# Performance work log

Measured on AMD Instinct MI355X. Metric: run time of the kernel, lower is better.

Reference implementation:

```python
import jax, jax.numpy as jnp
import numpy as np

B, T, H, C = 64, 2048, 128, 7


def _lstm_layer(xs, W_ih, W_hh, b):
    # xs: [T, B, H_in]; PyTorch gate order i, f, g, o
    Bsz = xs.shape[1]
    Hs = W_hh.shape[1]

    def step(carry, x_t):
        h, c = carry
        gates = x_t @ W_ih.T + h @ W_hh.T + b  # [B, 4H]
        i, f, g, o = jnp.split(gates, 4, axis=-1)
        c = jax.nn.sigmoid(f) * c + jax.nn.sigmoid(i) * jnp.tanh(g)
        h = jax.nn.sigmoid(o) * jnp.tanh(c)
        return (h, c), h

    init = (jnp.zeros((Bsz, Hs), xs.dtype), jnp.zeros((Bsz, Hs), xs.dtype))
    _, ys = jax.lax.scan(step, init, xs)
    return ys  # [T, B, H]


def setup_inputs() -> dict:
    key = jax.random.key(0)
    ks = jax.random.split(key, 12)
    s = 1.0 / np.sqrt(H)
    u = lambda k, shape: jax.random.uniform(k, shape, jnp.float32, -s, s)
    x = jax.random.normal(ks[0], (B, T, 1), jnp.float32)
    lengths = jax.random.randint(ks[1], (B,), 1, T + 1, jnp.int32)
    return {
        "x": x,
        "lengths": lengths,
        "ff_w": u(ks[2], (H, 1)),
        "ff_b": u(ks[3], (H,)),
        "W_ih0": u(ks[4], (4 * H, H)),
        "W_hh0": u(ks[5], (4 * H, H)),
        "b0": u(ks[6], (4 * H,)),  # b_ih + b_hh fused
        "W_ih1": u(ks[7], (4 * H, H)),
        "W_hh1": u(ks[8], (4 * H, H)),
        "b1": u(ks[9], (4 * H,)),
        "lin_w": u(ks[10], (C, 3 * H)),
        "lin_b": u(ks[11], (C,)),
    }


def reference(x, lengths, ff_w, ff_b, W_ih0, W_hh0, b0, W_ih1, W_hh1, b1, lin_w, lin_b):
    # input projection (Linear(1, H))
    xf = x @ ff_w.T + ff_b  # [B, T, H]
    xs = jnp.transpose(xf, (1, 0, 2))  # [T, B, H]
    h1 = _lstm_layer(xs, W_ih0, W_hh0, b0)
    h2 = _lstm_layer(h1, W_ih1, W_hh1, b1)
    out = jnp.transpose(h2, (1, 0, 2))  # [B, T, H]

    # masked mean / max / last pooling over valid timesteps
    mask = jnp.arange(T)[None, :] < lengths[:, None]  # [B, T]
    mf = mask[:, :, None].astype(out.dtype)
    mean = (out * mf).sum(axis=1) / lengths[:, None].astype(out.dtype)
    mx = jnp.max(jnp.where(mask[:, :, None], out, -jnp.inf), axis=1)
    idx = jnp.broadcast_to((lengths - 1)[:, None, None], (out.shape[0], 1, out.shape[2]))
    last = jnp.take_along_axis(out, idx, axis=1)[:, 0]
    h = jnp.concatenate([mean, mx, last], axis=-1)  # [B, 3H]
    return h @ lin_w.T + lin_b  # [B, C]
```

## Files before the change

kernel.cpp:

```cpp
#include <hip/hip_runtime.h>
#include <hip/hip_fp16.h>

#define TT 2048
#define BB 64
#define HH 128
#define GG 512
#define CH 64
#define NCH (TT / CH)

typedef _Float16 f16x8 __attribute__((ext_vector_type(8)));
typedef _Float16 f16x4 __attribute__((ext_vector_type(4)));
typedef float f32x4 __attribute__((ext_vector_type(4)));

__device__ __forceinline__ float sigm(float x) {
    return __builtin_amdgcn_rcpf(1.0f + __expf(-x));
}
__device__ __forceinline__ float tanh_f(float x) {
    return 1.0f - 2.0f * __builtin_amdgcn_rcpf(1.0f + __expf(2.0f * x));
}
__device__ __forceinline__ void bar_lds() {
    asm volatile("s_waitcnt lgkmcnt(0)\n\ts_barrier" ::: "memory");
}

__device__ __forceinline__ f16x8 load_frag(const float* rowp, int kt, int lh) {
    const float4* p4 = (const float4*)(rowp + kt * 32 + lh * 8);
    float4 a = p4[0], b = p4[1];
    f16x8 f;
    f[0] = (_Float16)a.x; f[1] = (_Float16)a.y; f[2] = (_Float16)a.z; f[3] = (_Float16)a.w;
    f[4] = (_Float16)b.x; f[5] = (_Float16)b.y; f[6] = (_Float16)b.z; f[7] = (_Float16)b.w;
    return f;
}

__global__ __launch_bounds__(512, 1) void k_pipe(
    const float* __restrict__ x, const int* __restrict__ lengths,
    const float* __restrict__ ff_w, const float* __restrict__ ff_b,
    const float* __restrict__ W_ih0, const float* __restrict__ W_hh0,
    const float* __restrict__ b0, const float* __restrict__ W_ih1,
    const float* __restrict__ W_hh1, const float* __restrict__ b1,
    _Float16* __restrict__ h0g, int* __restrict__ flags,
    float* __restrict__ pooled) {
    const int tid = threadIdx.x;
    const int w = tid >> 6;
    const int lane = tid & 63;
    const int c = lane & 15;
    const int lh = lane >> 4;
    const int un = 16 * w + c;
    const bool ard = (c == 0);
    const bool wr16 = (lane < 16);

    __shared__ float xs[TT];
    __shared__ _Float16 Hb0[2][HH];
    __shared__ _Float16 Hb1[2][HH];
    __shared__ _Float16 Qs[CH][GG];

    if (blockIdx.x < BB) {
        const int b = blockIdx.x;
        for (int i = tid; i < TT; i += 512) xs[i] = x[b * TT + i];
        if (tid < 2 * HH) ((_Float16*)Hb0)[tid] = (_Float16)0.f;

        f16x8 Bf[4][4];
        float v[4], u0[4];
#pragma unroll
        for (int t2 = 0; t2 < 4; ++t2) {
            const int r = t2 * HH + un;
#pragma unroll
            for (int kt = 0; kt < 4; ++kt) Bf[t2][kt] = load_frag(W_hh0 + r * HH, kt, lh);
            const float4* wi4 = (const float4*)(W_ih0 + r * HH);
            const float4* fw4 = (const float4*)ff_w;
            const float4* fb4 = (const float4*)ff_b;
            float vv = 0.f, uu = 0.f;
#pragma unroll
            for (int m = 0; m < HH / 4; ++m) {
                float4 a = wi4[m], fw = fw4[m], fb = fb4[m];
                vv += a.x * fw.x + a.y * fw.y + a.z * fw.z + a.w * fw.w;
                uu += a.x * fb.x + a.y * fb.y + a.z * fb.z + a.w * fb.w;
            }
            v[t2] = vv;
            u0[t2] = uu + b0[r];
        }
#pragma unroll
        for (int t2 = 0; t2 < 4; ++t2)
#pragma unroll
            for (int kt = 0; kt < 4; ++kt) asm volatile("" : "+v"(Bf[t2][kt]));

        float cst0 = 0.f;
        f16x8 av[4];
#pragma unroll
        for (int kt = 0; kt < 4; ++kt) av[kt] = (f16x8){0, 0, 0, 0, 0, 0, 0, 0};
        __syncthreads();

#define PSTEP(T_, RB_)                                                          \
    do {                                                                        \
        if (ard) {                                                              \
            _Pragma("unroll") for (int kt = 0; kt < 4; ++kt)                    \
                av[kt] = *(const f16x8*)&Hb0[RB_][kt * 32 + lh * 8];            \
        }                                                                       \
        const float xt = xs[T_];                                                \
        float p[4];                                                             \
        _Pragma("unroll") for (int t2 = 0; t2 < 4; ++t2) {                      \
            f32x4 alo, ahi;                                                     \
            const float ci = xt * v[t2] + u0[t2];                               \
            alo[0] = ci;  alo[1] = 0.f; alo[2] = 0.f; alo[3] = 0.f;             \
            ahi[0] = 0.f; ahi[1] = 0.f; ahi[2] = 0.f; ahi[3] = 0.f;             \
            alo = __builtin_amdgcn_mfma_f32_16x16x32_f16(av[0], Bf[t2][0],      \
                                                         alo, 0, 0, 0);         \
            ahi = __builtin_amdgcn_mfma_f32_16x16x32_f16(av[2], Bf[t2][2],      \
                                                         ahi, 0, 0, 0);         \
            alo = __builtin_amdgcn_mfma_f32_16x16x32_f16(av[1], Bf[t2][1],      \
                                                         alo, 0, 0, 0);         \
            ahi = __builtin_amdgcn_mfma_f32_16x16x32_f16(av[3], Bf[t2][3],      \
                                                         ahi, 0, 0, 0);         \
            p[t2] = alo[0] + ahi[0];                                            \
        }                                                                       \
        float gi = sigm(p[0]), gf = sigm(p[1]);                                 \
        float gg = tanh_f(p[2]), go = sigm(p[3]);                               \
        cst0 = gf * cst0 + gi * gg;                                             \
        float h0n = go * tanh_f(cst0);                                          \
        if (wr16) {                                                             \
            Hb0[(RB_) ^ 1][un] = (_Float16)h0n;                                 \
            __builtin_nontemporal_store(                                        \
                (_Float16)h0n, h0g + ((size_t)b * TT + (T_)) * HH + un);        \
        }                                                                       \
        bar_lds();                                                              \
    } while (0)

        for (int ch = 0; ch < NCH; ++ch) {
            const int t0 = ch * CH;
            for (int j = 0; j < CH; j += 2) {
                PSTEP(t0 + j, 0);
                PSTEP(t0 + j + 1, 1);
            }
            __syncthreads();
            if (tid == 0)
                __hip_atomic_store(&flags[b * NCH + ch], ch + 1, __ATOMIC_RELEASE,
                                   __HIP_MEMORY_SCOPE_AGENT);
        }
#undef PSTEP
    } else {
        const int b = blockIdx.x - BB;
        if (tid < 2 * HH) ((_Float16*)Hb1)[tid] = (_Float16)0.f;

        f16x8 Bh[4][4];
        float bb1[4];
#pragma unroll
        for (int t2 = 0; t2 < 4; ++t2) {
#pragma unroll
            for (int kt = 0; kt < 4; ++kt)
                Bh[t2][kt] = load_frag(W_hh1 + (t2 * HH + un) * HH, kt, lh);
            bb1[t2] = b1[t2 * HH + un];
        }
#pragma unroll
        for (int t2 = 0; t2 < 4; ++t2)
#pragma unroll
            for (int kt = 0; kt < 4; ++kt) asm volatile("" : "+v"(Bh[t2][kt]));

        const int len = lengths[b];
        float cst1 = 0.f, mean = 0.f, mx = -1e30f, last = 0.f;
        f16x8 av[4];
#pragma unroll
        for (int kt = 0; kt < 4; ++kt) av[kt] = (f16x8){0, 0, 0, 0, 0, 0, 0, 0};
        __syncthreads();

#define CSTEP(T_, RB_)                                                          \
    do {                                                                        \
        const int jj = (T_) & (CH - 1);                                         \
        f16x4 qv = *(const f16x4*)&Qs[jj][un * 4];    \
        if (ard) {                                                              \
            _Pragma("unroll") for (int kt = 0; kt < 4; ++kt)                    \
                av[kt] = *(const f16x8*)&Hb1[RB_][kt * 32 + lh * 8];            \
        }                                                                       \
        float p[4];                                                             \
        _Pragma("unroll") for (int t2 = 0; t2 < 4; ++t2) {                      \
            f32x4 alo, ahi;                                                     \
            alo[0] = (float)qv[t2];                                             \
            alo[1] = 0.f; alo[2] = 0.f; alo[3] = 0.f;                           \
            ahi[0] = 0.f; ahi[1] = 0.f; ahi[2] = 0.f; ahi[3] = 0.f;             \
            alo = __builtin_amdgcn_mfma_f32_16x16x32_f16(av[0], Bh[t2][0],      \
                                                         alo, 0, 0, 0);         \
            ahi = __builtin_amdgcn_mfma_f32_16x16x32_f16(av[2], Bh[t2][2],      \
                                                         ahi, 0, 0, 0);         \
            alo = __builtin_amdgcn_mfma_f32_16x16x32_f16(av[1], Bh[t2][1],      \
                                                         alo, 0, 0, 0);         \
            ahi = __builtin_amdgcn_mfma_f32_16x16x32_f16(av[3], Bh[t2][3],      \
                                                         ahi, 0, 0, 0);         \
            p[t2] = alo[0] + ahi[0];                                            \
        }                                                                       \
        float gi = sigm(p[0]), gf = sigm(p[1]);                                 \
        float gg = tanh_f(p[2]), go = sigm(p[3]);                               \
        cst1 = gf * cst1 + gi * gg;                                             \
        float h1n = go * tanh_f(cst1);                                          \
        if (wr16) Hb1[(RB_) ^ 1][un] = (_Float16)h1n;                           \
        if ((T_) < len) {                                                       \
            mean += h1n;                                                        \
            mx = fmaxf(mx, h1n);                                                \
        }                                                                       \
        if ((T_) == len - 1) last = h1n;                                        \
        bar_lds();                                                              \
    } while (0)

        for (int ch = 0; ch < NCH; ++ch) {
            if (tid == 0) {
                int guard = 0;
                while (__hip_atomic_load(&flags[b * NCH + ch], __ATOMIC_ACQUIRE,
                                         __HIP_MEMORY_SCOPE_AGENT) != ch + 1) {
                    __builtin_amdgcn_s_sleep(8);
                    if (++guard > (1 << 22)) break;
                }
            }
            __syncthreads();
            f16x8 Bi[4][4];
#pragma unroll
            for (int t2 = 0; t2 < 4; ++t2)
#pragma unroll
                for (int kt = 0; kt < 4; ++kt)
                    Bi[t2][kt] = load_frag(W_ih1 + (t2 * HH + un) * HH, kt, lh);
            const _Float16* hbase = h0g + ((size_t)b * TT + ch * CH) * HH;
#pragma unroll
            for (int mt = 0; mt < 4; ++mt) {
                f16x8 am[4];
#pragma unroll
                for (int kt = 0; kt < 4; ++kt)
                    am[kt] = *(const f16x8*)(hbase + (mt * 16 + c) * HH + kt * 32 + lh * 8);
                f32x4 qa[4];
#pragma unroll
                for (int t2 = 0; t2 < 4; ++t2) {
                    qa[t2] = (f32x4){0.f, 0.f, 0.f, 0.f};
#pragma unroll
                    for (int kt = 0; kt < 4; ++kt)
                        qa[t2] = __builtin_amdgcn_mfma_f32_16x16x32_f16(
                            am[kt], Bi[t2][kt], qa[t2], 0, 0, 0);
                }
#pragma unroll
                for (int r = 0; r < 4; ++r) {
                    f16x4 qv;
#pragma unroll
                    for (int t2 = 0; t2 < 4; ++t2) qv[t2] = (_Float16)(qa[t2][r] + bb1[t2]);
                    *(f16x4*)&Qs[mt * 16 + 4 * lh + r][un * 4] = qv;
                }
            }
            __syncthreads();
            const int t0 = ch * CH;
            for (int j = 0; j < CH; j += 2) {
                CSTEP(t0 + j, 0);
                CSTEP(t0 + j + 1, 1);
            }
        }
#undef CSTEP
        if (wr16) {
            pooled[b * 384 + un] = mean / (float)len;
            pooled[b * 384 + 128 + un] = mx;
            pooled[b * 384 + 256 + un] = last;
        }
    }
}

__global__ __launch_bounds__(448) void k_head(
    const float* __restrict__ pooled, const float* __restrict__ lin_w,
    const float* __restrict__ lin_b, float* __restrict__ out) {
    int tid = threadIdx.x;
    int b = tid / 7, cc = tid % 7;
    const float* p = pooled + b * 384;
    const float* wr = lin_w + cc * 384;
    float a0 = 0.f, a1 = 0.f, a2 = 0.f, a3 = 0.f;
#pragma unroll
    for (int k = 0; k < 384; k += 4) {
        a0 += p[k + 0] * wr[k + 0];
        a1 += p[k + 1] * wr[k + 1];
        a2 += p[k + 2] * wr[k + 2];
        a3 += p[k + 3] * wr[k + 3];
    }
    out[tid] = lin_b[cc] + ((a0 + a1) + (a2 + a3));
}

extern "C" void kernel_launch(void* const* d_in, const int* in_sizes, int n_in,
                              void* d_out, int out_size, void* d_ws, size_t ws_size,
                              hipStream_t stream) {
    const float* x     = (const float*)d_in[0];
    const int*   lens  = (const int*)d_in[1];
    const float* ff_w  = (const float*)d_in[2];
    const float* ff_b  = (const float*)d_in[3];
    const float* W_ih0 = (const float*)d_in[4];
    const float* W_hh0 = (const float*)d_in[5];
    const float* b0    = (const float*)d_in[6];
    const float* W_ih1 = (const float*)d_in[7];
    const float* W_hh1 = (const float*)d_in[8];
    const float* b1    = (const float*)d_in[9];
    const float* lin_w = (const float*)d_in[10];
    const float* lin_b = (const float*)d_in[11];
    float* out = (float*)d_out;

    char* ws = (char*)d_ws;
    const size_t HBYTES = (size_t)BB * TT * HH * 2;
    _Float16* h0g = (_Float16*)ws;
    int* flags    = (int*)(ws + HBYTES);
    float* pooled = (float*)(ws + HBYTES + 8192);

    k_pipe<<<dim3(2 * BB), dim3(512), 0, stream>>>(
        x, lens, ff_w, ff_b, W_ih0, W_hh0, b0, W_ih1, W_hh1, b1, h0g, flags, pooled);
    k_head<<<dim3(1), dim3(448), 0, stream>>>(pooled, lin_w, lin_b, out);
}
```

Measured before the change: 1.382 ms.

## Halve block size so each wave computes two hidden-unit tiles per step

Each block now runs 4 waves instead of 8, and every wave handles two 16-unit column tiles of the recurrent matmul and gate math. Fewer waves make the per-step LDS barrier cheaper on the serial time loop, while each wave does twice the MFMA and transcendental work and keeps twice the weight fragments in registers. The spin-wait on the producer flag also sleeps for shorter intervals and has a larger guard limit.

```diff
diff --git a/kernel.cpp b/kernel.cpp
--- a/kernel.cpp
+++ b/kernel.cpp
@@ -31,7 +31,7 @@
     return f;
 }
 
-__global__ __launch_bounds__(512, 1) void k_pipe(
+__global__ __launch_bounds__(256, 1) void k_pipe(
     const float* __restrict__ x, const int* __restrict__ lengths,
     const float* __restrict__ ff_w, const float* __restrict__ ff_b,
     const float* __restrict__ W_ih0, const float* __restrict__ W_hh0,
@@ -44,7 +44,8 @@
     const int lane = tid & 63;
     const int c = lane & 15;
     const int lh = lane >> 4;
-    const int un = 16 * w + c;
+    const int un0 = 32 * w + c;
+    const int un1 = un0 + 16;
     const bool ard = (c == 0);
     const bool wr16 = (lane < 16);
 
@@ -55,35 +56,40 @@
 
     if (blockIdx.x < BB) {
         const int b = blockIdx.x;
-        for (int i = tid; i < TT; i += 512) xs[i] = x[b * TT + i];
-        if (tid < 2 * HH) ((_Float16*)Hb0)[tid] = (_Float16)0.f;
-
-        f16x8 Bf[4][4];
-        float v[4], u0[4];
-#pragma unroll
-        for (int t2 = 0; t2 < 4; ++t2) {
-            const int r = t2 * HH + un;
-#pragma unroll
-            for (int kt = 0; kt < 4; ++kt) Bf[t2][kt] = load_frag(W_hh0 + r * HH, kt, lh);
-            const float4* wi4 = (const float4*)(W_ih0 + r * HH);
-            const float4* fw4 = (const float4*)ff_w;
-            const float4* fb4 = (const float4*)ff_b;
-            float vv = 0.f, uu = 0.f;
-#pragma unroll
-            for (int m = 0; m < HH / 4; ++m) {
-                float4 a = wi4[m], fw = fw4[m], fb = fb4[m];
-                vv += a.x * fw.x + a.y * fw.y + a.z * fw.z + a.w * fw.w;
-                uu += a.x * fb.x + a.y * fb.y + a.z * fb.z + a.w * fb.w;
-            }
-            v[t2] = vv;
-            u0[t2] = uu + b0[r];
-        }
-#pragma unroll
-        for (int t2 = 0; t2 < 4; ++t2)
-#pragma unroll
-            for (int kt = 0; kt < 4; ++kt) asm volatile("" : "+v"(Bf[t2][kt]));
-
-        float cst0 = 0.f;
+        for (int i = tid; i < TT; i += 256) xs[i] = x[b * TT + i];
+        ((_Float16*)Hb0)[tid] = (_Float16)0.f;
+
+        f16x8 Bf[2][4][4];
+        float v[2][4], u0[2][4];
+#pragma unroll
+        for (int tile = 0; tile < 2; ++tile)
+#pragma unroll
+            for (int t2 = 0; t2 < 4; ++t2) {
+                const int r = t2 * HH + 32 * w + 16 * tile + c;
+#pragma unroll
+                for (int kt = 0; kt < 4; ++kt)
+                    Bf[tile][t2][kt] = load_frag(W_hh0 + r * HH, kt, lh);
+                const float4* wi4 = (const float4*)(W_ih0 + r * HH);
+                const float4* fw4 = (const float4*)ff_w;
+                const float4* fb4 = (const float4*)ff_b;
+                float vv = 0.f, uu = 0.f;
+#pragma unroll
+                for (int m = 0; m < HH / 4; ++m) {
+                    float4 a = wi4[m], fw = fw4[m], fb = fb4[m];
+                    vv += a.x * fw.x + a.y * fw.y + a.z * fw.z + a.w * fw.w;
+                    uu += a.x * fb.x + a.y * fb.y + a.z * fb.z + a.w * fb.w;
+                }
+                v[tile][t2] = vv;
+                u0[tile][t2] = uu + b0[r];
+            }
+#pragma unroll
+        for (int tile = 0; tile < 2; ++tile)
+#pragma unroll
+            for (int t2 = 0; t2 < 4; ++t2)
+#pragma unroll
+                for (int kt = 0; kt < 4; ++kt) asm volatile("" : "+v"(Bf[tile][t2][kt]));
+
+        float cst[2] = {0.f, 0.f};
         f16x8 av[4];
 #pragma unroll
         for (int kt = 0; kt < 4; ++kt) av[kt] = (f16x8){0, 0, 0, 0, 0, 0, 0, 0};
@@ -96,30 +102,34 @@
                 av[kt] = *(const f16x8*)&Hb0[RB_][kt * 32 + lh * 8];            \
         }                                                                       \
         const float xt = xs[T_];                                                \
-        float p[4];                                                             \
+        float p[2][4];                                                          \
+        _Pragma("unroll") for (int tile = 0; tile < 2; ++tile)                  \
         _Pragma("unroll") for (int t2 = 0; t2 < 4; ++t2) {                      \
             f32x4 alo, ahi;                                                     \
-            const float ci = xt * v[t2] + u0[t2];                               \
+            const float ci = xt * v[tile][t2] + u0[tile][t2];                   \
             alo[0] = ci;  alo[1] = 0.f; alo[2] = 0.f; alo[3] = 0.f;             \
             ahi[0] = 0.f; ahi[1] = 0.f; ahi[2] = 0.f; ahi[3] = 0.f;             \
-            alo = __builtin_amdgcn_mfma_f32_16x16x32_f16(av[0], Bf[t2][0],      \
+            alo = __builtin_amdgcn_mfma_f32_16x16x32_f16(av[0], Bf[tile][t2][0],\
                                                          alo, 0, 0, 0);         \
-            ahi = __builtin_amdgcn_mfma_f32_16x16x32_f16(av[2], Bf[t2][2],      \
+            ahi = __builtin_amdgcn_mfma_f32_16x16x32_f16(av[2], Bf[tile][t2][2],\
                                                          ahi, 0, 0, 0);         \
-            alo = __builtin_amdgcn_mfma_f32_16x16x32_f16(av[1], Bf[t2][1],      \
+            alo = __builtin_amdgcn_mfma_f32_16x16x32_f16(av[1], Bf[tile][t2][1],\
                                                          alo, 0, 0, 0);         \
-            ahi = __builtin_amdgcn_mfma_f32_16x16x32_f16(av[3], Bf[t2][3],      \
+            ahi = __builtin_amdgcn_mfma_f32_16x16x32_f16(av[3], Bf[tile][t2][3],\
                                                          ahi, 0, 0, 0);         \
-            p[t2] = alo[0] + ahi[0];                                            \
-        }                                                                       \
-        float gi = sigm(p[0]), gf = sigm(p[1]);                                 \
-        float gg = tanh_f(p[2]), go = sigm(p[3]);                               \
-        cst0 = gf * cst0 + gi * gg;                                             \
-        float h0n = go * tanh_f(cst0);                                          \
-        if (wr16) {                                                             \
-            Hb0[(RB_) ^ 1][un] = (_Float16)h0n;                                 \
-            __builtin_nontemporal_store(                                        \
-                (_Float16)h0n, h0g + ((size_t)b * TT + (T_)) * HH + un);        \
+            p[tile][t2] = alo[0] + ahi[0];                                      \
+        }                                                                       \
+        _Pragma("unroll") for (int tile = 0; tile < 2; ++tile) {                \
+            float gi = sigm(p[tile][0]), gf = sigm(p[tile][1]);                 \
+            float gg = tanh_f(p[tile][2]), go = sigm(p[tile][3]);               \
+            cst[tile] = gf * cst[tile] + gi * gg;                               \
+            float h0n = go * tanh_f(cst[tile]);                                 \
+            if (wr16) {                                                         \
+                const int uu_ = un0 + 16 * tile;                                \
+                Hb0[(RB_) ^ 1][uu_] = (_Float16)h0n;                            \
+                __builtin_nontemporal_store(                                    \
+                    (_Float16)h0n, h0g + ((size_t)b * TT + (T_)) * HH + uu_);   \
+            }                                                                   \
         }                                                                       \
         bar_lds();                                                              \
     } while (0)
@@ -138,24 +148,30 @@
 #undef PSTEP
     } else {
         const int b = blockIdx.x - BB;
-        if (tid < 2 * HH) ((_Float16*)Hb1)[tid] = (_Float16)0.f;
-
-        f16x8 Bh[4][4];
-        float bb1[4];
-#pragma unroll
-        for (int t2 = 0; t2 < 4; ++t2) {
-#pragma unroll
-            for (int kt = 0; kt < 4; ++kt)
-                Bh[t2][kt] = load_frag(W_hh1 + (t2 * HH + un) * HH, kt, lh);
-            bb1[t2] = b1[t2 * HH + un];
-        }
-#pragma unroll
-        for (int t2 = 0; t2 < 4; ++t2)
-#pragma unroll
-            for (int kt = 0; kt < 4; ++kt) asm volatile("" : "+v"(Bh[t2][kt]));
+        ((_Float16*)Hb1)[tid] = (_Float16)0.f;
+
+        f16x8 Bh[2][4][4];
+        float bb1[2][4];
+#pragma unroll
+        for (int tile = 0; tile < 2; ++tile)
+#pragma unroll
+            for (int t2 = 0; t2 < 4; ++t2) {
+                const int r = t2 * HH + 32 * w + 16 * tile + c;
+#pragma unroll
+                for (int kt = 0; kt < 4; ++kt)
+                    Bh[tile][t2][kt] = load_frag(W_hh1 + r * HH, kt, lh);
+                bb1[tile][t2] = b1[r];
+            }
+#pragma unroll
+        for (int tile = 0; tile < 2; ++tile)
+#pragma unroll
+            for (int t2 = 0; t2 < 4; ++t2)
+#pragma unroll
+                for (int kt = 0; kt < 4; ++kt) asm volatile("" : "+v"(Bh[tile][t2][kt]));
 
         const int len = lengths[b];
-        float cst1 = 0.f, mean = 0.f, mx = -1e30f, last = 0.f;
+        float cst[2] = {0.f, 0.f};
+        float mean[2] = {0.f, 0.f}, mx[2] = {-1e30f, -1e30f}, last[2] = {0.f, 0.f};
         f16x8 av[4];
 #pragma unroll
         for (int kt = 0; kt < 4; ++kt) av[kt] = (f16x8){0, 0, 0, 0, 0, 0, 0, 0};
@@ -164,37 +180,41 @@
 #define CSTEP(T_, RB_)                                                          \
     do {                                                                        \
         const int jj = (T_) & (CH - 1);                                         \
-        f16x4 qv = *(const f16x4*)&Qs[jj][un * 4];    \
+        f16x4 qv0 = *(const f16x4*)&Qs[jj][un0 * 4];             \
+        f16x4 qv1 = *(const f16x4*)&Qs[jj][un1 * 4];                            \
         if (ard) {                                                              \
             _Pragma("unroll") for (int kt = 0; kt < 4; ++kt)                    \
                 av[kt] = *(const f16x8*)&Hb1[RB_][kt * 32 + lh * 8];            \
         }                                                                       \
-        float p[4];                                                             \
+        float p[2][4];                                                          \
+        _Pragma("unroll") for (int tile = 0; tile < 2; ++tile)                  \
         _Pragma("unroll") for (int t2 = 0; t2 < 4; ++t2) {                      \
             f32x4 alo, ahi;                                                     \
-            alo[0] = (float)qv[t2];                                             \
+            alo[0] = (float)(tile ? qv1[t2] : qv0[t2]);                         \
             alo[1] = 0.f; alo[2] = 0.f; alo[3] = 0.f;                           \
             ahi[0] = 0.f; ahi[1] = 0.f; ahi[2] = 0.f; ahi[3] = 0.f;             \
-            alo = __builtin_amdgcn_mfma_f32_16x16x32_f16(av[0], Bh[t2][0],      \
+            alo = __builtin_amdgcn_mfma_f32_16x16x32_f16(av[0], Bh[tile][t2][0],\
                                                          alo, 0, 0, 0);         \
-            ahi = __builtin_amdgcn_mfma_f32_16x16x32_f16(av[2], Bh[t2][2],      \
+            ahi = __builtin_amdgcn_mfma_f32_16x16x32_f16(av[2], Bh[tile][t2][2],\
                                                          ahi, 0, 0, 0);         \
-            alo = __builtin_amdgcn_mfma_f32_16x16x32_f16(av[1], Bh[t2][1],      \
+            alo = __builtin_amdgcn_mfma_f32_16x16x32_f16(av[1], Bh[tile][t2][1],\
                                                          alo, 0, 0, 0);         \
-            ahi = __builtin_amdgcn_mfma_f32_16x16x32_f16(av[3], Bh[t2][3],      \
+            ahi = __builtin_amdgcn_mfma_f32_16x16x32_f16(av[3], Bh[tile][t2][3],\
                                                          ahi, 0, 0, 0);         \
-            p[t2] = alo[0] + ahi[0];                                            \
-        }                                                                       \
-        float gi = sigm(p[0]), gf = sigm(p[1]);                                 \
-        float gg = tanh_f(p[2]), go = sigm(p[3]);                               \
-        cst1 = gf * cst1 + gi * gg;                                             \
-        float h1n = go * tanh_f(cst1);                                          \
-        if (wr16) Hb1[(RB_) ^ 1][un] = (_Float16)h1n;                           \
-        if ((T_) < len) {                                                       \
-            mean += h1n;                                                        \
-            mx = fmaxf(mx, h1n);                                                \
-        }                                                                       \
-        if ((T_) == len - 1) last = h1n;                                        \
+            p[tile][t2] = alo[0] + ahi[0];                                      \
+        }                                                                       \
+        _Pragma("unroll") for (int tile = 0; tile < 2; ++tile) {                \
+            float gi = sigm(p[tile][0]), gf = sigm(p[tile][1]);                 \
+            float gg = tanh_f(p[tile][2]), go = sigm(p[tile][3]);               \
+            cst[tile] = gf * cst[tile] + gi * gg;                               \
+            float h1n = go * tanh_f(cst[tile]);                                 \
+            if (wr16) Hb1[(RB_) ^ 1][un0 + 16 * tile] = (_Float16)h1n;          \
+            if ((T_) < len) {                                                   \
+                mean[tile] += h1n;                                              \
+                mx[tile] = fmaxf(mx[tile], h1n);                                \
+            }                                                                   \
+            if ((T_) == len - 1) last[tile] = h1n;                              \
+        }                                                                       \
         bar_lds();                                                              \
     } while (0)
 
@@ -203,39 +223,44 @@
                 int guard = 0;
                 while (__hip_atomic_load(&flags[b * NCH + ch], __ATOMIC_ACQUIRE,
                                          __HIP_MEMORY_SCOPE_AGENT) != ch + 1) {
-                    __builtin_amdgcn_s_sleep(8);
-                    if (++guard > (1 << 22)) break;
+                    __builtin_amdgcn_s_sleep(2);
+                    if (++guard > (1 << 24)) break;
                 }
             }
             __syncthreads();
-            f16x8 Bi[4][4];
-#pragma unroll
-            for (int t2 = 0; t2 < 4; ++t2)
-#pragma unroll
-                for (int kt = 0; kt < 4; ++kt)
-                    Bi[t2][kt] = load_frag(W_ih1 + (t2 * HH + un) * HH, kt, lh);
             const _Float16* hbase = h0g + ((size_t)b * TT + ch * CH) * HH;
 #pragma unroll
-            for (int mt = 0; mt < 4; ++mt) {
-                f16x8 am[4];
-#pragma unroll
-                for (int kt = 0; kt < 4; ++kt)
-                    am[kt] = *(const f16x8*)(hbase + (mt * 16 + c) * HH + kt * 32 + lh * 8);
-                f32x4 qa[4];
-#pragma unroll
-                for (int t2 = 0; t2 < 4; ++t2) {
-                    qa[t2] = (f32x4){0.f, 0.f, 0.f, 0.f};
+            for (int tile = 0; tile < 2; ++tile) {
+                f16x8 Bi[4][4];
+#pragma unroll
+                for (int t2 = 0; t2 < 4; ++t2)
 #pragma unroll
                     for (int kt = 0; kt < 4; ++kt)
-                        qa[t2] = __builtin_amdgcn_mfma_f32_16x16x32_f16(
-                            am[kt], Bi[t2][kt], qa[t2], 0, 0, 0);
-                }
-#pragma unroll
-                for (int r = 0; r < 4; ++r) {
-                    f16x4 qv;
-#pragma unroll
-                    for (int t2 = 0; t2 < 4; ++t2) qv[t2] = (_Float16)(qa[t2][r] + bb1[t2]);
-                    *(f16x4*)&Qs[mt * 16 + 4 * lh + r][un * 4] = qv;
+                        Bi[t2][kt] = load_frag(
+                            W_ih1 + (t2 * HH + 32 * w + 16 * tile + c) * HH, kt, lh);
+#pragma unroll
+                for (int mt = 0; mt < 4; ++mt) {
+                    f16x8 am[4];
+#pragma unroll
+                    for (int kt = 0; kt < 4; ++kt)
+                        am[kt] = *(const f16x8*)(hbase + (mt * 16 + c) * HH + kt * 32 + lh * 8);
+                    f32x4 qa[4];
+#pragma unroll
+                    for (int t2 = 0; t2 < 4; ++t2) {
+                        qa[t2] = (f32x4){0.f, 0.f, 0.f, 0.f};
+#pragma unroll
+                        for (int kt = 0; kt < 4; ++kt)
+                            qa[t2] = __builtin_amdgcn_mfma_f32_16x16x32_f16(
+                                am[kt], Bi[t2][kt], qa[t2], 0, 0, 0);
+                    }
+#pragma unroll
+                    for (int r = 0; r < 4; ++r) {
+                        f16x4 qv;
+#pragma unroll
+                        for (int t2 = 0; t2 < 4; ++t2)
+                            qv[t2] = (_Float16)(qa[t2][r] + bb1[tile][t2]);
+                        *(f16x4*)&Qs[mt * 16 + 4 * lh + r][(un0 + 16 * tile) * 4] = qv;
+                    }
                 }
             }
             __syncthreads();
@@ -247,9 +272,13 @@
         }
 #undef CSTEP
         if (wr16) {
-            pooled[b * 384 + un] = mean / (float)len;
-            pooled[b * 384 + 128 + un] = mx;
-            pooled[b * 384 + 256 + un] = last;
+#pragma unroll
+            for (int tile = 0; tile < 2; ++tile) {
+                const int uu_ = un0 + 16 * tile;
+                pooled[b * 384 + uu_] = mean[tile] / (float)len;
+                pooled[b * 384 + 128 + uu_] = mx[tile];
+                pooled[b * 384 + 256 + uu_] = last[tile];
+            }
         }
     }
 }
@@ -295,7 +324,7 @@
     int* flags    = (int*)(ws + HBYTES);
     float* pooled = (float*)(ws + HBYTES + 8192);
 
-    k_pipe<<<dim3(2 * BB), dim3(512), 0, stream>>>(
+    k_pipe<<<dim3(2 * BB), dim3(256), 0, stream>>>(
         x, lens, ff_w, ff_b, W_ih0, W_hh0, b0, W_ih1, W_hh1, b1, h0g, flags, pooled);
     k_head<<<dim3(1), dim3(448), 0, stream>>>(pooled, lin_w, lin_b, out);
 }
```

Measured after the change: 1.657 ms. +19.9%, slower.

## Process two batch sequences per block to interleave independent recurrences

Applied to the files above, without the earlier changes.

Each block now runs the LSTM recurrence for two batch elements at once, so the grid shrinks from 128 to 64 blocks. The two independent dependency chains are interleaved inside each step: two sets of MFMAs, two sets of gate math, and one shared barrier per step. The aim is to hide MFMA and transcendental latency and to amortise the per-step barrier and LDS round trip across two sequences. The cost is twice the work on each serial chain, more registers and LDS, and half as many CUs in use.

```diff
diff --git a/kernel.cpp b/kernel.cpp
--- a/kernel.cpp
+++ b/kernel.cpp
@@ -3,6 +3,7 @@
 
 #define TT 2048
 #define BB 64
+#define PB 32
 #define HH 128
 #define GG 512
 #define CH 64
@@ -48,15 +49,19 @@
     const bool ard = (c == 0);
     const bool wr16 = (lane < 16);
 
-    __shared__ float xs[TT];
-    __shared__ _Float16 Hb0[2][HH];
-    __shared__ _Float16 Hb1[2][HH];
-    __shared__ _Float16 Qs[CH][GG];
-
-    if (blockIdx.x < BB) {
-        const int b = blockIdx.x;
-        for (int i = tid; i < TT; i += 512) xs[i] = x[b * TT + i];
-        if (tid < 2 * HH) ((_Float16*)Hb0)[tid] = (_Float16)0.f;
+    __shared__ float xs[2][TT];
+    __shared__ _Float16 Hb0[2][2][HH];
+    __shared__ _Float16 Hb1[2][2][HH];
+    __shared__ _Float16 Qs[2][CH][GG];
+
+    if (blockIdx.x < PB) {
+        const int pb = blockIdx.x;
+        const int bA = 2 * pb, bB = 2 * pb + 1;
+        for (int i = tid; i < TT; i += 512) {
+            xs[0][i] = x[bA * TT + i];
+            xs[1][i] = x[bB * TT + i];
+        }
+        ((_Float16*)Hb0)[tid] = (_Float16)0.f;
 
         f16x8 Bf[4][4];
         float v[4], u0[4];
@@ -83,43 +88,70 @@
 #pragma unroll
             for (int kt = 0; kt < 4; ++kt) asm volatile("" : "+v"(Bf[t2][kt]));
 
-        float cst0 = 0.f;
-        f16x8 av[4];
-#pragma unroll
-        for (int kt = 0; kt < 4; ++kt) av[kt] = (f16x8){0, 0, 0, 0, 0, 0, 0, 0};
+        float cstA = 0.f, cstB = 0.f;
+        f16x8 avA[4], avB[4];
+#pragma unroll
+        for (int kt = 0; kt < 4; ++kt) {
+            avA[kt] = (f16x8){0, 0, 0, 0, 0, 0, 0, 0};
+            avB[kt] = (f16x8){0, 0, 0, 0, 0, 0, 0, 0};
+        }
         __syncthreads();
 
-#define PSTEP(T_, RB_)                                                          \
+#define PSTEP2(T_, RB_)                                                         \
     do {                                                                        \
         if (ard) {                                                              \
             _Pragma("unroll") for (int kt = 0; kt < 4; ++kt)                    \
-                av[kt] = *(const f16x8*)&Hb0[RB_][kt * 32 + lh * 8];            \
-        }                                                                       \
-        const float xt = xs[T_];                                                \
-        float p[4];                                                             \
+                avA[kt] = *(const f16x8*)&Hb0[0][RB_][kt * 32 + lh * 8];        \
+            _Pragma("unroll") for (int kt = 0; kt < 4; ++kt)                    \
+                avB[kt] = *(const f16x8*)&Hb0[1][RB_][kt * 32 + lh * 8];        \
+        }                                                                       \
+        const float xtA = xs[0][T_], xtB = xs[1][T_];                           \
+        float pA[4], pB[4];                                                     \
         _Pragma("unroll") for (int t2 = 0; t2 < 4; ++t2) {                      \
             f32x4 alo, ahi;                                                     \
-            const float ci = xt * v[t2] + u0[t2];                               \
+            const float ci = xtA * v[t2] + u0[t2];                              \
             alo[0] = ci;  alo[1] = 0.f; alo[2] = 0.f; alo[3] = 0.f;             \
             ahi[0] = 0.f; ahi[1] = 0.f; ahi[2] = 0.f; ahi[3] = 0.f;             \
-            alo = __builtin_amdgcn_mfma_f32_16x16x32_f16(av[0], Bf[t2][0],      \
-                                                         alo, 0, 0, 0);         \
-            ahi = __builtin_amdgcn_mfma_f32_16x16x32_f16(av[2], Bf[t2][2],      \
-                                                         ahi, 0, 0, 0);         \
-            alo = __builtin_amdgcn_mfma_f32_16x16x32_f16(av[1], Bf[t2][1],      \
-                                                         alo, 0, 0, 0);         \
-            ahi = __builtin_amdgcn_mfma_f32_16x16x32_f16(av[3], Bf[t2][3],      \
-                                                         ahi, 0, 0, 0);         \
-            p[t2] = alo[0] + ahi[0];                                            \
-        }                                                                       \
-        float gi = sigm(p[0]), gf = sigm(p[1]);                                 \
-        float gg = tanh_f(p[2]), go = sigm(p[3]);                               \
-        cst0 = gf * cst0 + gi * gg;                                             \
-        float h0n = go * tanh_f(cst0);                                          \
+            alo = __builtin_amdgcn_mfma_f32_16x16x32_f16(avA[0], Bf[t2][0],     \
+                                                         alo, 0, 0, 0);         \
+            ahi = __builtin_amdgcn_mfma_f32_16x16x32_f16(avA[2], Bf[t2][2],     \
+                                                         ahi, 0, 0, 0);         \
+            alo = __builtin_amdgcn_mfma_f32_16x16x32_f16(avA[1], Bf[t2][1],     \
+                                                         alo, 0, 0, 0);         \
+            ahi = __builtin_amdgcn_mfma_f32_16x16x32_f16(avA[3], Bf[t2][3],     \
+                                                         ahi, 0, 0, 0);         \
+            pA[t2] = alo[0] + ahi[0];                                           \
+        }                                                                       \
+        _Pragma("unroll") for (int t2 = 0; t2 < 4; ++t2) {                      \
+            f32x4 alo, ahi;                                                     \
+            const float ci = xtB * v[t2] + u0[t2];                              \
+            alo[0] = ci;  alo[1] = 0.f; alo[2] = 0.f; alo[3] = 0.f;             \
+            ahi[0] = 0.f; ahi[1] = 0.f; ahi[2] = 0.f; ahi[3] = 0.f;             \
+            alo = __builtin_amdgcn_mfma_f32_16x16x32_f16(avB[0], Bf[t2][0],     \
+                                                         alo, 0, 0, 0);         \
+            ahi = __builtin_amdgcn_mfma_f32_16x16x32_f16(avB[2], Bf[t2][2],     \
+                                                         ahi, 0, 0, 0);         \
+            alo = __builtin_amdgcn_mfma_f32_16x16x32_f16(avB[1], Bf[t2][1],     \
+                                                         alo, 0, 0, 0);         \
+            ahi = __builtin_amdgcn_mfma_f32_16x16x32_f16(avB[3], Bf[t2][3],     \
+                                                         ahi, 0, 0, 0);         \
+            pB[t2] = alo[0] + ahi[0];                                           \
+        }                                                                       \
+        float giA = sigm(pA[0]), gfA = sigm(pA[1]);                             \
+        float giB = sigm(pB[0]), gfB = sigm(pB[1]);                             \
+        float ggA = tanh_f(pA[2]), goA = sigm(pA[3]);                           \
+        float ggB = tanh_f(pB[2]), goB = sigm(pB[3]);                           \
+        cstA = gfA * cstA + giA * ggA;                                          \
+        cstB = gfB * cstB + giB * ggB;                                          \
+        float hA = goA * tanh_f(cstA);                                          \
+        float hB = goB * tanh_f(cstB);                                          \
         if (wr16) {                                                             \
-            Hb0[(RB_) ^ 1][un] = (_Float16)h0n;                                 \
+            Hb0[0][(RB_) ^ 1][un] = (_Float16)hA;                               \
+            Hb0[1][(RB_) ^ 1][un] = (_Float16)hB;                               \
             __builtin_nontemporal_store(                                        \
-                (_Float16)h0n, h0g + ((size_t)b * TT + (T_)) * HH + un);        \
+                (_Float16)hA, h0g + ((size_t)bA * TT + (T_)) * HH + un);        \
+            __builtin_nontemporal_store(                                        \
+                (_Float16)hB, h0g + ((size_t)bB * TT + (T_)) * HH + un);        \
         }                                                                       \
         bar_lds();                                                              \
     } while (0)
@@ -127,18 +159,19 @@
         for (int ch = 0; ch < NCH; ++ch) {
             const int t0 = ch * CH;
             for (int j = 0; j < CH; j += 2) {
-                PSTEP(t0 + j, 0);
-                PSTEP(t0 + j + 1, 1);
+                PSTEP2(t0 + j, 0);
+                PSTEP2(t0 + j + 1, 1);
             }
             __syncthreads();
             if (tid == 0)
-                __hip_atomic_store(&flags[b * NCH + ch], ch + 1, __ATOMIC_RELEASE,
+                __hip_atomic_store(&flags[pb * NCH + ch], ch + 1, __ATOMIC_RELEASE,
                                    __HIP_MEMORY_SCOPE_AGENT);
         }
-#undef PSTEP
+#undef PSTEP2
     } else {
-        const int b = blockIdx.x - BB;
-        if (tid < 2 * HH) ((_Float16*)Hb1)[tid] = (_Float16)0.f;
+        const int pb = blockIdx.x - PB;
+        const int bA = 2 * pb, bB = 2 * pb + 1;
+        ((_Float16*)Hb1)[tid] = (_Float16)0.f;
 
         f16x8 Bh[4][4];
         float bb1[4];
@@ -154,54 +187,83 @@
 #pragma unroll
             for (int kt = 0; kt < 4; ++kt) asm volatile("" : "+v"(Bh[t2][kt]));
 
-        const int len = lengths[b];
-        float cst1 = 0.f, mean = 0.f, mx = -1e30f, last = 0.f;
-        f16x8 av[4];
-#pragma unroll
-        for (int kt = 0; kt < 4; ++kt) av[kt] = (f16x8){0, 0, 0, 0, 0, 0, 0, 0};
+        const int lenA = lengths[bA], lenB = lengths[bB];
+        float cstA = 0.f, cstB = 0.f;
+        float meanA = 0.f, mxA = -1e30f, lastA = 0.f;
+        float meanB = 0.f, mxB = -1e30f, lastB = 0.f;
+        f16x8 avA[4], avB[4];
+#pragma unroll
+        for (int kt = 0; kt < 4; ++kt) {
+            avA[kt] = (f16x8){0, 0, 0, 0, 0, 0, 0, 0};
+            avB[kt] = (f16x8){0, 0, 0, 0, 0, 0, 0, 0};
+        }
         __syncthreads();
 
-#define CSTEP(T_, RB_)                                                          \
+#define CSTEP2(T_, RB_)                                                         \
     do {                                                                        \
         const int jj = (T_) & (CH - 1);                                         \
-        f16x4 qv = *(const f16x4*)&Qs[jj][un * 4];    \
+        f16x4 qvA = *(const f16x4*)&Qs[0][jj][un * 4];           \
+        f16x4 qvB = *(const f16x4*)&Qs[1][jj][un * 4];                          \
         if (ard) {                                                              \
             _Pragma("unroll") for (int kt = 0; kt < 4; ++kt)                    \
-                av[kt] = *(const f16x8*)&Hb1[RB_][kt * 32 + lh * 8];            \
-        }                                                                       \
-        float p[4];                                                             \
+                avA[kt] = *(const f16x8*)&Hb1[0][RB_][kt * 32 + lh * 8];        \
+            _Pragma("unroll") for (int kt = 0; kt < 4; ++kt)                    \
+                avB[kt] = *(const f16x8*)&Hb1[1][RB_][kt * 32 + lh * 8];        \
+        }                                                                       \
+        float pA[4], pB[4];                                                     \
         _Pragma("unroll") for (int t2 = 0; t2 < 4; ++t2) {                      \
             f32x4 alo, ahi;                                                     \
-            alo[0] = (float)qv[t2];                                             \
+            alo[0] = (float)qvA[t2];                                            \
             alo[1] = 0.f; alo[2] = 0.f; alo[3] = 0.f;                           \
             ahi[0] = 0.f; ahi[1] = 0.f; ahi[2] = 0.f; ahi[3] = 0.f;             \
-            alo = __builtin_amdgcn_mfma_f32_16x16x32_f16(av[0], Bh[t2][0],      \
-                                                         alo, 0, 0, 0);         \
-            ahi = __builtin_amdgcn_mfma_f32_16x16x32_f16(av[2], Bh[t2][2],      \
-                                                         ahi, 0, 0, 0);         \
-            alo = __builtin_amdgcn_mfma_f32_16x16x32_f16(av[1], Bh[t2][1],      \
-                                                         alo, 0, 0, 0);         \
-            ahi = __builtin_amdgcn_mfma_f32_16x16x32_f16(av[3], Bh[t2][3],      \
-                                                         ahi, 0, 0, 0);         \
-            p[t2] = alo[0] + ahi[0];                                            \
-        }                                                                       \
-        float gi = sigm(p[0]), gf = sigm(p[1]);                                 \
-        float gg = tanh_f(p[2]), go = sigm(p[3]);                               \
-        cst1 = gf * cst1 + gi * gg;                                             \
-        float h1n = go * tanh_f(cst1);                                          \
-        if (wr16) Hb1[(RB_) ^ 1][un] = (_Float16)h1n;                           \
-        if ((T_) < len) {                                                       \
-            mean += h1n;                                                        \
-            mx = fmaxf(mx, h1n);                                                \
-        }                                                                       \
-        if ((T_) == len - 1) last = h1n;                                        \
+            alo = __builtin_amdgcn_mfma_f32_16x16x32_f16(avA[0], Bh[t2][0],     \
+                                                         alo, 0, 0, 0);         \
+            ahi = __builtin_amdgcn_mfma_f32_16x16x32_f16(avA[2], Bh[t2][2],     \
+                                                         ahi, 0, 0, 0);         \
+            alo = __builtin_amdgcn_mfma_f32_16x16x32_f16(avA[1], Bh[t2][1],     \
+                                                         alo, 0, 0, 0);         \
+            ahi = __builtin_amdgcn_mfma_f32_16x16x32_f16(avA[3], Bh[t2][3],     \
+                                                         ahi, 0, 0, 0);         \
+            pA[t2] = alo[0] + ahi[0];                                           \
+        }                                                                       \
+        _Pragma("unroll") for (int t2 = 0; t2 < 4; ++t2) {                      \
+            f32x4 alo, ahi;                                                     \
+            alo[0] = (float)qvB[t2];                                            \
+            alo[1] = 0.f; alo[2] = 0.f; alo[3] = 0.f;                           \
+            ahi[0] = 0.f; ahi[1] = 0.f; ahi[2] = 0.f; ahi[3] = 0.f;             \
+            alo = __builtin_amdgcn_mfma_f32_16x16x32_f16(avB[0], Bh[t2][0],     \
+                                                         alo, 0, 0, 0);         \
+            ahi = __builtin_amdgcn_mfma_f32_16x16x32_f16(avB[2], Bh[t2][2],     \
+                                                         ahi, 0, 0, 0);         \
+            alo = __builtin_amdgcn_mfma_f32_16x16x32_f16(avB[1], Bh[t2][1],     \
+                                                         alo, 0, 0, 0);         \
+            ahi = __builtin_amdgcn_mfma_f32_16x16x32_f16(avB[3], Bh[t2][3],     \
+                                                         ahi, 0, 0, 0);         \
+            pB[t2] = alo[0] + ahi[0];                                           \
+        }                                                                       \
+        float giA = sigm(pA[0]), gfA = sigm(pA[1]);                             \
+        float giB = sigm(pB[0]), gfB = sigm(pB[1]);                             \
+        float ggA = tanh_f(pA[2]), goA = sigm(pA[3]);                           \
+        float ggB = tanh_f(pB[2]), goB = sigm(pB[3]);                           \
+        cstA = gfA * cstA + giA * ggA;                                          \
+        cstB = gfB * cstB + giB * ggB;                                          \
+        float hA = goA * tanh_f(cstA);                                          \
+        float hB = goB * tanh_f(cstB);                                          \
+        if (wr16) {                                                             \
+            Hb1[0][(RB_) ^ 1][un] = (_Float16)hA;                               \
+            Hb1[1][(RB_) ^ 1][un] = (_Float16)hB;                               \
+        }                                                                       \
+        if ((T_) < lenA) { meanA += hA; mxA = fmaxf(mxA, hA); }                 \
+        if ((T_) == lenA - 1) lastA = hA;                                       \
+        if ((T_) < lenB) { meanB += hB; mxB = fmaxf(mxB, hB); }                 \
+        if ((T_) == lenB - 1) lastB = hB;                                       \
         bar_lds();                                                              \
     } while (0)
 
         for (int ch = 0; ch < NCH; ++ch) {
             if (tid == 0) {
                 int guard = 0;
-                while (__hip_atomic_load(&flags[b * NCH + ch], __ATOMIC_ACQUIRE,
+                while (__hip_atomic_load(&flags[pb * NCH + ch], __ATOMIC_ACQUIRE,
                                          __HIP_MEMORY_SCOPE_AGENT) != ch + 1) {
                     __builtin_amdgcn_s_sleep(8);
                     if (++guard > (1 << 22)) break;
@@ -214,42 +276,49 @@
 #pragma unroll
                 for (int kt = 0; kt < 4; ++kt)
                     Bi[t2][kt] = load_frag(W_ih1 + (t2 * HH + un) * HH, kt, lh);
-            const _Float16* hbase = h0g + ((size_t)b * TT + ch * CH) * HH;
-#pragma unroll
-            for (int mt = 0; mt < 4; ++mt) {
-                f16x8 am[4];
-#pragma unroll
-                for (int kt = 0; kt < 4; ++kt)
-                    am[kt] = *(const f16x8*)(hbase + (mt * 16 + c) * HH + kt * 32 + lh * 8);
-                f32x4 qa[4];
-#pragma unroll
-                for (int t2 = 0; t2 < 4; ++t2) {
-                    qa[t2] = (f32x4){0.f, 0.f, 0.f, 0.f};
+#pragma unroll
+            for (int bt = 0; bt < 2; ++bt) {
+                const _Float16* hbase =
+                    h0g + ((size_t)(2 * pb + bt) * TT + ch * CH) * HH;
+#pragma unroll
+                for (int mt = 0; mt < 4; ++mt) {
+                    f16x8 am[4];
 #pragma unroll
                     for (int kt = 0; kt < 4; ++kt)
-                        qa[t2] = __builtin_amdgcn_mfma_f32_16x16x32_f16(
-                            am[kt], Bi[t2][kt], qa[t2], 0, 0, 0);
-                }
-#pragma unroll
-                for (int r = 0; r < 4; ++r) {
-                    f16x4 qv;
-#pragma unroll
-                    for (int t2 = 0; t2 < 4; ++t2) qv[t2] = (_Float16)(qa[t2][r] + bb1[t2]);
-                    *(f16x4*)&Qs[mt * 16 + 4 * lh + r][un * 4] = qv;
+                        am[kt] = *(const f16x8*)(hbase + (mt * 16 + c) * HH + kt * 32 + lh * 8);
+                    f32x4 qa[4];
+#pragma unroll
+                    for (int t2 = 0; t2 < 4; ++t2) {
+                        qa[t2] = (f32x4){0.f, 0.f, 0.f, 0.f};
+#pragma unroll
+                        for (int kt = 0; kt < 4; ++kt)
+                            qa[t2] = __builtin_amdgcn_mfma_f32_16x16x32_f16(
+                                am[kt], Bi[t2][kt], qa[t2], 0, 0, 0);
+                    }
+#pragma unroll
+                    for (int r = 0; r < 4; ++r) {
+                        f16x4 qv;
+#pragma unroll
+                        for (int t2 = 0; t2 < 4; ++t2) qv[t2] = (_Float16)(qa[t2][r] + bb1[t2]);
+                        *(f16x4*)&Qs[bt][mt * 16 + 4 * lh + r][un * 4] = qv;
+                    }
                 }
             }
             __syncthreads();
             const int t0 = ch * CH;
             for (int j = 0; j < CH; j += 2) {
-                CSTEP(t0 + j, 0);
-                CSTEP(t0 + j + 1, 1);
-            }
-        }
-#undef CSTEP
+                CSTEP2(t0 + j, 0);
+                CSTEP2(t0 + j + 1, 1);
+            }
+        }
+#undef CSTEP2
         if (wr16) {
-            pooled[b * 384 + un] = mean / (float)len;
-            pooled[b * 384 + 128 + un] = mx;
-            pooled[b * 384 + 256 + un] = last;
+            pooled[bA * 384 + un] = meanA / (float)lenA;
+            pooled[bA * 384 + 128 + un] = mxA;
+            pooled[bA * 384 + 256 + un] = lastA;
+            pooled[bB * 384 + un] = meanB / (float)lenB;
+            pooled[bB * 384 + 128 + un] = mxB;
+            pooled[bB * 384 + 256 + un] = lastB;
         }
     }
 }
@@ -295,7 +364,7 @@
     int* flags    = (int*)(ws + HBYTES);
     float* pooled = (float*)(ws + HBYTES + 8192);
 
-    k_pipe<<<dim3(2 * BB), dim3(512), 0, stream>>>(
+    k_pipe<<<dim3(2 * PB), dim3(512), 0, stream>>>(
         x, lens, ff_w, ff_b, W_ih0, W_hh0, b0, W_ih1, W_hh1, b1, h0g, flags, pooled);
     k_head<<<dim3(1), dim3(448), 0, stream>>>(pooled, lin_w, lin_b, out);
 }
```

New measurement: 2.439 ms. 76.5% more time.
